# Kernel tuning notes

Hardware: AMD Instinct MI355X
Metric: run time of the kernel (lower is better)

The kernel has to match this reference:

```python
import jax, jax.numpy as jnp
import numpy as np

N = 100000       # nodes
E0 = 1600000     # random edges (self-loops appended -> E = E0 + N)
IN = 128         # input feature dim
H1, C1 = 8, 8    # conv1 heads, out channels per head
C2 = 64          # num_classes (conv2 out, heads=1)
NEG_SLOPE = 0.2


def gat_conv(x, src, dst, W, att_src, att_dst, bias, heads, out_ch, concat):
    """PyG-style GATConv (eval mode, no dropout). x: [N, F_in]."""
    n = x.shape[0]
    h = (x @ W).reshape(n, heads, out_ch)              # [N, H, C]
    a_src = jnp.sum(h * att_src, axis=-1)              # [N, H]
    a_dst = jnp.sum(h * att_dst, axis=-1)              # [N, H]
    e = jax.nn.leaky_relu(a_src[src] + a_dst[dst], NEG_SLOPE)  # [E, H]
    # segment softmax over edges grouped by destination node
    e_max = jax.ops.segment_max(e, dst, num_segments=n)
    ex = jnp.exp(e - e_max[dst])
    denom = jax.ops.segment_sum(ex, dst, num_segments=n)
    alpha = ex / denom[dst]                            # [E, H]
    msg = h[src] * alpha[:, :, None]                   # [E, H, C]
    out = jax.ops.segment_sum(msg, dst, num_segments=n)  # [N, H, C]
    out = out.reshape(n, heads * out_ch) if concat else out.mean(axis=1)
    return out + bias


def setup_inputs() -> dict:
    key = jax.random.key(0)
    ks = jax.random.split(key, 12)
    nodes = jnp.arange(N, dtype=jnp.int32)
    feat = jax.random.normal(ks[0], (N, IN), jnp.float32)
    src = jax.random.randint(ks[1], (E0,), 0, N, jnp.int32)
    dst = jax.random.randint(ks[2], (E0,), 0, N, jnp.int32)
    loop = jnp.arange(N, dtype=jnp.int32)
    edge_index = jnp.stack([jnp.concatenate([src, loop]),
                            jnp.concatenate([dst, loop])])  # [2, E]
    mask = jnp.ones((N,), bool)
    label = jax.random.randint(ks[3], (N,), 0, C2, jnp.int32)
    s = 0.1
    W1 = jax.random.normal(ks[4], (IN, H1 * C1), jnp.float32) * s
    att_src1 = jax.random.normal(ks[5], (H1, C1), jnp.float32) * s
    att_dst1 = jax.random.normal(ks[6], (H1, C1), jnp.float32) * s
    b1 = jnp.zeros((H1 * C1,), jnp.float32)
    W2 = jax.random.normal(ks[7], (H1 * C1, C2), jnp.float32) * s
    att_src2 = jax.random.normal(ks[8], (1, C2), jnp.float32) * s
    att_dst2 = jax.random.normal(ks[9], (1, C2), jnp.float32) * s
    b2 = jnp.zeros((C2,), jnp.float32)
    return {"nodes": nodes, "feat": feat, "edge_index": edge_index, "mask": mask,
            "label": label, "W1": W1, "att_src1": att_src1, "att_dst1": att_dst1,
            "b1": b1, "W2": W2, "att_src2": att_src2, "att_dst2": att_dst2, "b2": b2}


def reference(nodes, feat, edge_index, mask, label,
              W1, att_src1, att_dst1, b1, W2, att_src2, att_dst2, b2):
    src, dst = edge_index[0], edge_index[1]
    x = jax.nn.elu(gat_conv(feat, src, dst, W1, att_src1, att_dst1, b1,
                            H1, C1, concat=True))          # [N, 64]
    scores = gat_conv(x, src, dst, W2, att_src2, att_dst2, b2,
                      1, C2, concat=False)                  # [N, C2]
    logp = jax.nn.log_softmax(scores, axis=-1)
    nll = -jnp.take_along_axis(logp, label[:, None].astype(jnp.int32), axis=1)[:, 0]
    m = mask.astype(scores.dtype)
    loss = jnp.sum(nll * m) / jnp.sum(m)                    # masked mean CE
    pred = jnp.argmax(scores, axis=1)
    return loss, pred, label
```

## Files before the change

kernel.cpp:

```cpp
#include <hip/hip_runtime.h>
#include <cstdint>

#define NHEAD 8
#define D1 64
#define IN_F 128
#define NEG 0.2f
#define NBINS 256
#define BINS 1024
#define BSH 7
#define CHUNK 8192

__device__ __forceinline__ void fma4(float4& a, float s, const float4& v)
{
    a.x = fmaf(s, v.x, a.x); a.y = fmaf(s, v.y, a.y);
    a.z = fmaf(s, v.z, a.z); a.w = fmaf(s, v.w, a.w);
}

__global__ __launch_bounds__(256) void k_gemm1_hist(
    const float* __restrict__ feat,
    const float* __restrict__ W1,
    const float* __restrict__ att_s,
    const float* __restrict__ att_d,
    float* __restrict__ h1, float* __restrict__ a_src, float* __restrict__ a_dst,
    const int* __restrict__ dst, int* __restrict__ btot, int* __restrict__ bh,
    int N, int E, int GH)
{
    __shared__ float Wh[32 * 64];
    __shared__ float Fh[64 * 36];
    const int tid = threadIdx.x;

    if ((int)blockIdx.x < GH) {
        int* hist = (int*)Wh;
        for (int b = tid; b < BINS; b += 256) hist[b] = 0;
        __syncthreads();
        const int e0 = blockIdx.x * CHUNK;
        #pragma unroll
        for (int r = 0; r < 8; ++r) {
            int e = e0 + r * 1024 + tid * 4;
            if (e + 3 < E) {
                int4 d4 = *(const int4*)&dst[e];
                atomicAdd(&hist[d4.x >> BSH], 1);
                atomicAdd(&hist[d4.y >> BSH], 1);
                atomicAdd(&hist[d4.z >> BSH], 1);
                atomicAdd(&hist[d4.w >> BSH], 1);
            } else {
                for (int k = e; k < E && k < e + 4; ++k)
                    atomicAdd(&hist[dst[k] >> BSH], 1);
            }
        }
        __syncthreads();
        for (int b = tid; b < BINS; b += 256) {
            int c = hist[b];
            bh[(size_t)blockIdx.x * BINS + b] = c;
            if (c) atomicAdd(&btot[b * 16], c);
        }
        return;
    }

    const int tx = tid & 15, ty = tid >> 4;
    const int base = (blockIdx.x - GH) * 64;
    float4 acc0 = {0,0,0,0}, acc1 = {0,0,0,0}, acc2 = {0,0,0,0}, acc3 = {0,0,0,0};

    for (int p = 0; p < 4; ++p) {
        if (p) __syncthreads();
        for (int i = tid; i < 32 * 64; i += 256)
            Wh[i] = W1[p * 2048 + i];
        for (int i = tid; i < 64 * 32; i += 256) {
            int r = i >> 5, kk = i & 31;
            int n = base + r;
            Fh[r * 36 + kk] = (n < N) ? feat[(size_t)n * IN_F + p * 32 + kk] : 0.f;
        }
        __syncthreads();
        const float* wk = &Wh[4 * tx];
        const float* f0 = &Fh[(4 * ty + 0) * 36];
        const float* f1 = &Fh[(4 * ty + 1) * 36];
        const float* f2 = &Fh[(4 * ty + 2) * 36];
        const float* f3 = &Fh[(4 * ty + 3) * 36];
        #pragma unroll
        for (int kk = 0; kk < 32; kk += 4) {
            float4 fa = *(const float4*)&f0[kk];
            float4 fb = *(const float4*)&f1[kk];
            float4 fc = *(const float4*)&f2[kk];
            float4 fd = *(const float4*)&f3[kk];
            float4 w0 = *(const float4*)&wk[(kk + 0) * 64];
            float4 w1 = *(const float4*)&wk[(kk + 1) * 64];
            float4 w2 = *(const float4*)&wk[(kk + 2) * 64];
            float4 w3 = *(const float4*)&wk[(kk + 3) * 64];
            fma4(acc0, fa.x, w0); fma4(acc0, fa.y, w1); fma4(acc0, fa.z, w2); fma4(acc0, fa.w, w3);
            fma4(acc1, fb.x, w0); fma4(acc1, fb.y, w1); fma4(acc1, fb.z, w2); fma4(acc1, fb.w, w3);
            fma4(acc2, fc.x, w0); fma4(acc2, fc.y, w1); fma4(acc2, fc.z, w2); fma4(acc2, fc.w, w3);
            fma4(acc3, fd.x, w0); fma4(acc3, fd.y, w1); fma4(acc3, fd.z, w2); fma4(acc3, fd.w, w3);
        }
    }
    const float4 as4 = *(const float4*)&att_s[4 * tx];
    const float4 ad4 = *(const float4*)&att_d[4 * tx];
    float4 accs[4] = {acc0, acc1, acc2, acc3};
    #pragma unroll
    for (int i = 0; i < 4; ++i) {
        int n = base + 4 * ty + i;
        if (n < N) {
            *(float4*)&h1[(size_t)n * D1 + 4 * tx] = accs[i];
            float ps = accs[i].x * as4.x + accs[i].y * as4.y + accs[i].z * as4.z + accs[i].w * as4.w;
            float pd = accs[i].x * ad4.x + accs[i].y * ad4.y + accs[i].z * ad4.z + accs[i].w * ad4.w;
            ps += __shfl_xor(ps, 1);
            pd += __shfl_xor(pd, 1);
            if ((tx & 1) == 0) {
                a_src[n * NHEAD + (tx >> 1)] = ps;
                a_dst[n * NHEAD + (tx >> 1)] = pd;
            }
        }
    }
}

__device__ __forceinline__ int block_incl_scan(int v, int tid, int* lds4)
{
    int lane = tid & 63, w = tid >> 6;
    #pragma unroll
    for (int off = 1; off < 64; off <<= 1) {
        int t = __shfl_up(v, off);
        if (lane >= off) v += t;
    }
    if (lane == 63) lds4[w] = v;
    __syncthreads();
    int add = 0;
    #pragma unroll
    for (int i = 0; i < 4; ++i)
        if (i < w) add += lds4[i];
    __syncthreads();
    return v + add;
}

__global__ __launch_bounds__(256) void k_bscan(
    const int* __restrict__ btot, int* __restrict__ bbase, int* __restrict__ gcur,
    double* __restrict__ bins)
{
    __shared__ int lds4[4];
    const int tid = threadIdx.x;
    bins[tid] = 0.0;
    int c0 = btot[(4 * tid + 0) * 16];
    int c1 = btot[(4 * tid + 1) * 16];
    int c2 = btot[(4 * tid + 2) * 16];
    int c3 = btot[(4 * tid + 3) * 16];
    int v = c0 + c1 + c2 + c3;
    int incl = block_incl_scan(v, tid, lds4);
    int b0 = incl - v, b1 = b0 + c0, b2 = b1 + c1, b3 = b2 + c2;
    bbase[4 * tid + 0] = b0; gcur[(4 * tid + 0) * 16] = b0;
    bbase[4 * tid + 1] = b1; gcur[(4 * tid + 1) * 16] = b1;
    bbase[4 * tid + 2] = b2; gcur[(4 * tid + 2) * 16] = b2;
    bbase[4 * tid + 3] = b3; gcur[(4 * tid + 3) * 16] = b3;
}

__global__ __launch_bounds__(256) void k_scatter(
    const int* __restrict__ src, const int* __restrict__ dst,
    const int* __restrict__ bh, int* __restrict__ gcur,
    int* __restrict__ bucketed, int E)
{
    __shared__ int base[BINS], cur[BINS];
    const int tid = threadIdx.x;
    for (int b = tid; b < BINS; b += 256) {
        cur[b] = 0;
        int c = bh[(size_t)blockIdx.x * BINS + b];
        if (c) base[b] = atomicAdd(&gcur[b * 16], c);
    }
    __syncthreads();
    const int e0 = blockIdx.x * CHUNK;
    #pragma unroll
    for (int r = 0; r < 8; ++r) {
        int e = e0 + r * 1024 + tid * 4;
        if (e + 3 < E) {
            int4 d4 = *(const int4*)&dst[e];
            int4 s4 = *(const int4*)&src[e];
            int bx, rx;
            bx = d4.x >> BSH; rx = atomicAdd(&cur[bx], 1); bucketed[base[bx] + rx] = ((d4.x & 127) << 17) | s4.x;
            bx = d4.y >> BSH; rx = atomicAdd(&cur[bx], 1); bucketed[base[bx] + rx] = ((d4.y & 127) << 17) | s4.y;
            bx = d4.z >> BSH; rx = atomicAdd(&cur[bx], 1); bucketed[base[bx] + rx] = ((d4.z & 127) << 17) | s4.z;
            bx = d4.w >> BSH; rx = atomicAdd(&cur[bx], 1); bucketed[base[bx] + rx] = ((d4.w & 127) << 17) | s4.w;
        } else {
            for (int k = e; k < E && k < e + 4; ++k) {
                int d = dst[k];
                int bx = d >> BSH;
                int rx = atomicAdd(&cur[bx], 1);
                bucketed[base[bx] + rx] = ((d & 127) << 17) | src[k];
            }
        }
    }
}

__global__ __launch_bounds__(256) void k_seg(
    const int* __restrict__ btot, const int* __restrict__ bbase,
    const int* __restrict__ bucketed,
    int* __restrict__ deg, int* __restrict__ rowstart, int* __restrict__ srcs, int N)
{
    __shared__ int cnt[128], cur[128], lb[128];
    const int tid = threadIdx.x;
    const int b = blockIdx.x;
    const int gs = bbase[b];
    const int sz = btot[b * 16];
    if (tid < 128) { cnt[tid] = 0; cur[tid] = 0; }
    __syncthreads();
    for (int i = tid; i < sz; i += 256)
        atomicAdd(&cnt[bucketed[gs + i] >> 17], 1);
    __syncthreads();
    if (tid < 128) lb[tid] = cnt[tid];
    __syncthreads();
    #pragma unroll
    for (int off = 1; off < 128; off <<= 1) {
        int t = 0;
        if (tid < 128 && tid >= off) t = lb[tid - off];
        __syncthreads();
        if (tid < 128 && tid >= off) lb[tid] += t;
        __syncthreads();
    }
    if (tid < 128) {
        int ex = lb[tid] - cnt[tid];
        lb[tid] = ex;
        int d = b * 128 + tid;
        if (d < N) { deg[d] = cnt[tid]; rowstart[d] = gs + ex; }
    }
    __syncthreads();
    for (int i = tid; i < sz; i += 256) {
        int v = bucketed[gs + i];
        int d7 = v >> 17;
        int r = atomicAdd(&cur[d7], 1);
        srcs[gs + lb[d7] + r] = v & 0x1FFFF;
    }
}

__global__ __launch_bounds__(256) void k_agg1(
    const int* __restrict__ deg, const int* __restrict__ rowstart,
    const int* __restrict__ srcs,
    const float* __restrict__ a_s, const float* __restrict__ a_d,
    const float* __restrict__ h1, const float* __restrict__ b1,
    float* __restrict__ x, int N)
{
    __shared__ float sex[4][128];
    const int tid = threadIdx.x, w = tid >> 6, j = tid & 63;
    const int t = j & 15, q = j >> 4;
    const int n = blockIdx.x * 4 + w;
    if (n >= N) return;
    const int rlen = deg[n];
    const int row = rowstart[n];
    const float2 ad2 = *(const float2*)&a_d[n * NHEAD + 2 * q];
    const int h = t >> 1;
    float* sw = sex[w];
    float4 acc = {0.f, 0.f, 0.f, 0.f};
    float den = 0.f;
    bool v = (t < rlen);
    int   s  = v ? srcs[row + t] : 0;
    float2 a2 = v ? *(const float2*)&a_s[s * NHEAD + 2 * q] : make_float2(0.f, 0.f);
    for (int base = 0; base < rlen; base += 16) {
        bool vn = (base + 16 + t < rlen);
        int   sn  = vn ? srcs[row + base + 16 + t] : 0;
        float2 an = vn ? *(const float2*)&a_s[sn * NHEAD + 2 * q] : make_float2(0.f, 0.f);
        float e0 = 0.f, e1 = 0.f;
        if (v) {
            float x0 = a2.x + ad2.x; x0 = x0 > 0.f ? x0 : NEG * x0; e0 = __expf(x0);
            float x1 = a2.y + ad2.y; x1 = x1 > 0.f ? x1 : NEG * x1; e1 = __expf(x1);
        }
        *(float2*)&sw[t * 8 + 2 * q] = make_float2(e0, e1);
        asm volatile("s_waitcnt lgkmcnt(0)" ::: "memory");
        int mTot = rlen - base;
        if (4 * q < mTot) {
            int s0 = __shfl(s, 4 * q + 0), s1 = __shfl(s, 4 * q + 1);
            int s2 = __shfl(s, 4 * q + 2), s3 = __shfl(s, 4 * q + 3);
            float w0 = sw[(4 * q + 0) * 8 + h], w1 = sw[(4 * q + 1) * 8 + h];
            float w2 = sw[(4 * q + 2) * 8 + h], w3 = sw[(4 * q + 3) * 8 + h];
            float4 l0 = *(const float4*)&h1[(size_t)s0 * D1 + 4 * t];
            float4 l1 = *(const float4*)&h1[(size_t)s1 * D1 + 4 * t];
            float4 l2 = *(const float4*)&h1[(size_t)s2 * D1 + 4 * t];
            float4 l3 = *(const float4*)&h1[(size_t)s3 * D1 + 4 * t];
            fma4(acc, w0, l0); fma4(acc, w1, l1);
            fma4(acc, w2, l2); fma4(acc, w3, l3);
            den += (w0 + w1) + (w2 + w3);
        }
        asm volatile("s_waitcnt lgkmcnt(0)" ::: "memory");
        v = vn; s = sn; a2 = an;
    }
    acc.x += __shfl_xor(acc.x, 16); acc.y += __shfl_xor(acc.y, 16);
    acc.z += __shfl_xor(acc.z, 16); acc.w += __shfl_xor(acc.w, 16);
    den   += __shfl_xor(den, 16);
    acc.x += __shfl_xor(acc.x, 32); acc.y += __shfl_xor(acc.y, 32);
    acc.z += __shfl_xor(acc.z, 32); acc.w += __shfl_xor(acc.w, 32);
    den   += __shfl_xor(den, 32);
    if (q == 0) {
        float4 b = *(const float4*)&b1[4 * t];
        float4 o;
        o.x = acc.x / den + b.x; o.y = acc.y / den + b.y;
        o.z = acc.z / den + b.z; o.w = acc.w / den + b.w;
        o.x = o.x > 0.f ? o.x : expm1f(o.x);
        o.y = o.y > 0.f ? o.y : expm1f(o.y);
        o.z = o.z > 0.f ? o.z : expm1f(o.z);
        o.w = o.w > 0.f ? o.w : expm1f(o.w);
        *(float4*)&x[(size_t)n * D1 + 4 * t] = o;
    }
}

__global__ __launch_bounds__(256) void k_gemm2(
    const float* __restrict__ x,
    const float* __restrict__ W2,
    const float* __restrict__ att_s,
    const float* __restrict__ att_d,
    float* __restrict__ h2, float* __restrict__ a_src, float* __restrict__ a_dst,
    int N)
{
    __shared__ float Wh[64 * 64];
    __shared__ float Fh[64 * 68];
    const int tid = threadIdx.x;
    const int tx = tid & 15, ty = tid >> 4;
    const int base = blockIdx.x * 64;
    for (int i = tid; i < 64 * 64; i += 256)
        Wh[i] = W2[i];
    for (int i = tid; i < 64 * 64; i += 256) {
        int r = i >> 6, kk = i & 63;
        int n = base + r;
        Fh[r * 68 + kk] = (n < N) ? x[(size_t)n * 64 + kk] : 0.f;
    }
    __syncthreads();
    float4 acc0 = {0,0,0,0}, acc1 = {0,0,0,0}, acc2 = {0,0,0,0}, acc3 = {0,0,0,0};
    const float* wk = &Wh[4 * tx];
    const float* f0 = &Fh[(4 * ty + 0) * 68];
    const float* f1 = &Fh[(4 * ty + 1) * 68];
    const float* f2 = &Fh[(4 * ty + 2) * 68];
    const float* f3 = &Fh[(4 * ty + 3) * 68];
    #pragma unroll 4
    for (int kk = 0; kk < 64; kk += 4) {
        float4 fa = *(const float4*)&f0[kk];
        float4 fb = *(const float4*)&f1[kk];
        float4 fc = *(const float4*)&f2[kk];
        float4 fd = *(const float4*)&f3[kk];
        float4 w0 = *(const float4*)&wk[(kk + 0) * 64];
        float4 w1 = *(const float4*)&wk[(kk + 1) * 64];
        float4 w2 = *(const float4*)&wk[(kk + 2) * 64];
        float4 w3 = *(const float4*)&wk[(kk + 3) * 64];
        fma4(acc0, fa.x, w0); fma4(acc0, fa.y, w1); fma4(acc0, fa.z, w2); fma4(acc0, fa.w, w3);
        fma4(acc1, fb.x, w0); fma4(acc1, fb.y, w1); fma4(acc1, fb.z, w2); fma4(acc1, fb.w, w3);
        fma4(acc2, fc.x, w0); fma4(acc2, fc.y, w1); fma4(acc2, fc.z, w2); fma4(acc2, fc.w, w3);
        fma4(acc3, fd.x, w0); fma4(acc3, fd.y, w1); fma4(acc3, fd.z, w2); fma4(acc3, fd.w, w3);
    }
    const float4 as4 = *(const float4*)&att_s[4 * tx];
    const float4 ad4 = *(const float4*)&att_d[4 * tx];
    float4 accs[4] = {acc0, acc1, acc2, acc3};
    #pragma unroll
    for (int i = 0; i < 4; ++i) {
        int n = base + 4 * ty + i;
        if (n < N) {
            *(float4*)&h2[(size_t)n * 64 + 4 * tx] = accs[i];
            float ps = accs[i].x * as4.x + accs[i].y * as4.y + accs[i].z * as4.z + accs[i].w * as4.w;
            float pd = accs[i].x * ad4.x + accs[i].y * ad4.y + accs[i].z * ad4.z + accs[i].w * ad4.w;
            ps += __shfl_xor(ps, 1); pd += __shfl_xor(pd, 1);
            ps += __shfl_xor(ps, 2); pd += __shfl_xor(pd, 2);
            ps += __shfl_xor(ps, 4); pd += __shfl_xor(pd, 4);
            ps += __shfl_xor(ps, 8); pd += __shfl_xor(pd, 8);
            if (tx == 0) { a_src[n] = ps; a_dst[n] = pd; }
        }
    }
}

__global__ __launch_bounds__(256) void k_agg2(
    const int* __restrict__ deg, const int* __restrict__ rowstart,
    const int* __restrict__ srcs,
    const float* __restrict__ a_s, const float* __restrict__ a_d,
    const float* __restrict__ h2, const float* __restrict__ b2,
    const int* __restrict__ label,
    float* __restrict__ dout, double* __restrict__ bins, int N)
{
    __shared__ int2 sx[4][64];
    __shared__ float snll[16];
    const int tid = threadIdx.x, w = tid >> 6, j = tid & 63;
    const int t = j & 15, g16 = j & 0x30;
    const int n = blockIdx.x * 16 + (tid >> 4);
    if (tid < 16) snll[tid] = 0.f;
    __syncthreads();
    const bool valid = (n < N);
    const int rlen = valid ? deg[n] : 0;
    const int row  = valid ? rowstart[n] : 0;
    const float ad = valid ? a_d[n] : 0.f;
    float4 acc = {0.f, 0.f, 0.f, 0.f};
    float den = 0.f;
    for (int base = 0; base < rlen; base += 16) {
        int m = rlen - base; if (m > 16) m = 16;
        int myS = 0; float ex = 0.f;
        if (t < m) {
            myS = srcs[row + base + t];
            float v = a_s[myS] + ad;
            v = v > 0.f ? v : NEG * v;
            ex = __expf(v);
        }
        float ds = ex;
        ds += __shfl_xor(ds, 1); ds += __shfl_xor(ds, 2);
        ds += __shfl_xor(ds, 4); ds += __shfl_xor(ds, 8);
        den += ds;
        sx[w][j] = make_int2(myS, __float_as_int(ex));
        asm volatile("s_waitcnt lgkmcnt(0)" ::: "memory");
        for (int kb = 0; kb < m; kb += 4) {
            int2 p0 = sx[w][g16 | (kb + 0)];
            int2 p1 = sx[w][g16 | (kb + 1)];
            int2 p2 = sx[w][g16 | (kb + 2)];
            int2 p3 = sx[w][g16 | (kb + 3)];
            float4 l0 = *(const float4*)&h2[(size_t)p0.x * 64 + 4 * t];
            float4 l1 = *(const float4*)&h2[(size_t)p1.x * 64 + 4 * t];
            float4 l2 = *(const float4*)&h2[(size_t)p2.x * 64 + 4 * t];
            float4 l3 = *(const float4*)&h2[(size_t)p3.x * 64 + 4 * t];
            fma4(acc, __int_as_float(p0.y), l0);
            fma4(acc, __int_as_float(p1.y), l1);
            fma4(acc, __int_as_float(p2.y), l2);
            fma4(acc, __int_as_float(p3.y), l3);
        }
        asm volatile("s_waitcnt lgkmcnt(0)" ::: "memory");
    }
    float4 b = *(const float4*)&b2[4 * t];
    float4 sc;
    sc.x = acc.x / den + b.x; sc.y = acc.y / den + b.y;
    sc.z = acc.z / den + b.z; sc.w = acc.w / den + b.w;
    float mv = sc.x; int mi = 4 * t;
    if (sc.y > mv) { mv = sc.y; mi = 4 * t + 1; }
    if (sc.z > mv) { mv = sc.z; mi = 4 * t + 2; }
    if (sc.w > mv) { mv = sc.w; mi = 4 * t + 3; }
    #pragma unroll
    for (int off = 1; off < 16; off <<= 1) {
        float ov = __shfl_xor(mv, off);
        int oi = __shfl_xor(mi, off);
        if (ov > mv || (ov == mv && oi < mi)) { mv = ov; mi = oi; }
    }
    float se = __expf(sc.x - mv) + __expf(sc.y - mv) + __expf(sc.z - mv) + __expf(sc.w - mv);
    #pragma unroll
    for (int off = 1; off < 16; off <<= 1) se += __shfl_xor(se, off);
    int lab = valid ? label[n] : 0;
    int comp = lab & 3;
    float cl = comp == 0 ? sc.x : comp == 1 ? sc.y : comp == 2 ? sc.z : sc.w;
    float sl = __shfl(cl, g16 | (lab >> 2));
    if (t == 0 && valid) {
        snll[tid >> 4] = mv + logf(se) - sl;
        dout[1 + n] = (float)mi;
        dout[1 + (size_t)N + n] = (float)lab;
    }
    __syncthreads();
    if (tid == 0) {
        double bs = 0.0;
        #pragma unroll
        for (int i = 0; i < 16; ++i) bs += (double)snll[i];
        atomicAdd(&bins[blockIdx.x & (NBINS - 1)], bs);
    }
}

__global__ __launch_bounds__(256) void k_loss(
    const double* __restrict__ bins, float* __restrict__ dout, int N)
{
    __shared__ double sw[4];
    const int tid = threadIdx.x;
    double v = bins[tid];
    #pragma unroll
    for (int off = 1; off < 64; off <<= 1) v += __shfl_xor(v, off);
    if ((tid & 63) == 0) sw[tid >> 6] = v;
    __syncthreads();
    if (tid == 0)
        dout[0] = (float)((sw[0] + sw[1] + sw[2] + sw[3]) / (double)N);
}

extern "C" void kernel_launch(void* const* d_in, const int* in_sizes, int n_in,
                              void* d_out, int out_size, void* d_ws, size_t ws_size,
                              hipStream_t stream)
{
    const float* feat   = (const float*)d_in[1];
    const int*   edge   = (const int*)d_in[2];
    const int*   label  = (const int*)d_in[4];
    const float* W1     = (const float*)d_in[5];
    const float* att_s1 = (const float*)d_in[6];
    const float* att_d1 = (const float*)d_in[7];
    const float* b1     = (const float*)d_in[8];
    const float* W2     = (const float*)d_in[9];
    const float* att_s2 = (const float*)d_in[10];
    const float* att_d2 = (const float*)d_in[11];
    const float* b2     = (const float*)d_in[12];

    const int N = in_sizes[0];
    const int E = in_sizes[2] / 2;
    const int* src = edge;
    const int* dst = edge + E;

    float* bufA = (float*)d_ws;
    float* bufB = bufA + (size_t)N * 64;
    float* a_s1 = bufB + (size_t)N * 64;
    float* a_d1 = a_s1 + (size_t)N * 8;
    int*   deg  = (int*)(a_d1 + (size_t)N * 8);
    int*   rowstart = deg + N;
    int*   srcs = rowstart + N;
    double* bins = (double*)(((uintptr_t)(srcs + E) + 7) & ~(uintptr_t)7);

    int* bucketed = (int*)bufB;
    int* btot  = bucketed + E;
    int* gcur  = btot + BINS * 16;
    int* bbase = gcur + BINS * 16;
    int* bh    = bbase + BINS;

    float* a_s2 = a_s1;
    float* a_d2 = a_s1 + N;

    float* out = (float*)d_out;

    const int GH    = (E + CHUNK - 1) / CHUNK;
    const int G1    = (N + 63) / 64;
    const int NBUCK = (N + 127) / 128;

    hipMemsetAsync(btot, 0, (size_t)BINS * 16 * sizeof(int), stream);

    k_gemm1_hist<<<GH + G1, 256, 0, stream>>>(feat, W1, att_s1, att_d1,
                                              bufA, a_s1, a_d1,
                                              dst, btot, bh, N, E, GH);
    k_bscan  <<<1, 256, 0, stream>>>(btot, bbase, gcur, bins);
    k_scatter<<<GH, 256, 0, stream>>>(src, dst, bh, gcur, bucketed, E);
    k_seg    <<<NBUCK, 256, 0, stream>>>(btot, bbase, bucketed, deg, rowstart, srcs, N);

    k_agg1 <<<(N + 3) / 4, 256, 0, stream>>>(deg, rowstart, srcs, a_s1, a_d1,
                                             bufA, b1, bufB, N);
    k_gemm2<<<G1, 256, 0, stream>>>(bufB, W2, att_s2, att_d2, bufA, a_s2, a_d2, N);
    k_agg2 <<<(N + 15) / 16, 256, 0, stream>>>(deg, rowstart, srcs, a_s2, a_d2,
                                               bufA, b2, label, out, bins, N);
    k_loss <<<1, 256, 0, stream>>>(bins, out, N);
}
```

Measured before the change: 390.3 us.

## Spread GEMM1 tiles across CSR-build kernels and simplify agg1 weight computation

The layer-1 GEMM tiles are split into four portions and fused into the histogram, bucket-scan, scatter and segment kernels as extra blocks. The single-block scan and the atomic-bound sort stages then share the GPU with compute work instead of leaving CUs idle. Separately, k_agg1 drops the LDS-staged, software-prefetched exp weights and has each lane load its sources and compute its own exp directly. This removes LDS traffic and waitcnt barriers but adds redundant a_s loads and exp work per lane, and loses the prefetch pipelining.

```diff
diff --git a/kernel.cpp b/kernel.cpp
--- a/kernel.cpp
+++ b/kernel.cpp
@@ -16,49 +16,18 @@
     a.z = fmaf(s, v.z, a.z); a.w = fmaf(s, v.w, a.w);
 }
 
-__global__ __launch_bounds__(256) void k_gemm1_hist(
-    const float* __restrict__ feat,
-    const float* __restrict__ W1,
-    const float* __restrict__ att_s,
-    const float* __restrict__ att_d,
+__device__ __forceinline__ void gemm1_tile(
+    int gb,
+    const float* __restrict__ feat, const float* __restrict__ W1,
+    const float* __restrict__ att_s, const float* __restrict__ att_d,
     float* __restrict__ h1, float* __restrict__ a_src, float* __restrict__ a_dst,
-    const int* __restrict__ dst, int* __restrict__ btot, int* __restrict__ bh,
-    int N, int E, int GH)
+    int N)
 {
     __shared__ float Wh[32 * 64];
     __shared__ float Fh[64 * 36];
     const int tid = threadIdx.x;
-
-    if ((int)blockIdx.x < GH) {
-        int* hist = (int*)Wh;
-        for (int b = tid; b < BINS; b += 256) hist[b] = 0;
-        __syncthreads();
-        const int e0 = blockIdx.x * CHUNK;
-        #pragma unroll
-        for (int r = 0; r < 8; ++r) {
-            int e = e0 + r * 1024 + tid * 4;
-            if (e + 3 < E) {
-                int4 d4 = *(const int4*)&dst[e];
-                atomicAdd(&hist[d4.x >> BSH], 1);
-                atomicAdd(&hist[d4.y >> BSH], 1);
-                atomicAdd(&hist[d4.z >> BSH], 1);
-                atomicAdd(&hist[d4.w >> BSH], 1);
-            } else {
-                for (int k = e; k < E && k < e + 4; ++k)
-                    atomicAdd(&hist[dst[k] >> BSH], 1);
-            }
-        }
-        __syncthreads();
-        for (int b = tid; b < BINS; b += 256) {
-            int c = hist[b];
-            bh[(size_t)blockIdx.x * BINS + b] = c;
-            if (c) atomicAdd(&btot[b * 16], c);
-        }
-        return;
-    }
-
     const int tx = tid & 15, ty = tid >> 4;
-    const int base = (blockIdx.x - GH) * 64;
+    const int base = gb * 64;
     float4 acc0 = {0,0,0,0}, acc1 = {0,0,0,0}, acc2 = {0,0,0,0}, acc3 = {0,0,0,0};
 
     for (int p = 0; p < 4; ++p) {
@@ -112,6 +81,44 @@
     }
 }
 
+__global__ __launch_bounds__(256) void k_hist_g1(
+    const float* __restrict__ feat, const float* __restrict__ W1,
+    const float* __restrict__ att_s, const float* __restrict__ att_d,
+    float* __restrict__ h1, float* __restrict__ a_src, float* __restrict__ a_dst,
+    const int* __restrict__ dst, int* __restrict__ btot, int* __restrict__ bh,
+    int N, int E, int GH)
+{
+    const int tid = threadIdx.x;
+    if ((int)blockIdx.x < GH) {
+        __shared__ int hist[BINS];
+        for (int b = tid; b < BINS; b += 256) hist[b] = 0;
+        __syncthreads();
+        const int e0 = blockIdx.x * CHUNK;
+        #pragma unroll
+        for (int r = 0; r < 8; ++r) {
+            int e = e0 + r * 1024 + tid * 4;
+            if (e + 3 < E) {
+                int4 d4 = *(const int4*)&dst[e];
+                atomicAdd(&hist[d4.x >> BSH], 1);
+                atomicAdd(&hist[d4.y >> BSH], 1);
+                atomicAdd(&hist[d4.z >> BSH], 1);
+                atomicAdd(&hist[d4.w >> BSH], 1);
+            } else {
+                for (int k = e; k < E && k < e + 4; ++k)
+                    atomicAdd(&hist[dst[k] >> BSH], 1);
+            }
+        }
+        __syncthreads();
+        for (int b = tid; b < BINS; b += 256) {
+            int c = hist[b];
+            bh[(size_t)blockIdx.x * BINS + b] = c;
+            if (c) atomicAdd(&btot[b * 16], c);
+        }
+        return;
+    }
+    gemm1_tile(blockIdx.x - GH, feat, W1, att_s, att_d, h1, a_src, a_dst, N);
+}
+
 __device__ __forceinline__ int block_incl_scan(int v, int tid, int* lds4)
 {
     int lane = tid & 63, w = tid >> 6;
@@ -130,100 +137,122 @@
     return v + add;
 }
 
-__global__ __launch_bounds__(256) void k_bscan(
+__global__ __launch_bounds__(256) void k_bscan_g1(
+    const float* __restrict__ feat, const float* __restrict__ W1,
+    const float* __restrict__ att_s, const float* __restrict__ att_d,
+    float* __restrict__ h1, float* __restrict__ a_src, float* __restrict__ a_dst,
     const int* __restrict__ btot, int* __restrict__ bbase, int* __restrict__ gcur,
-    double* __restrict__ bins)
-{
-    __shared__ int lds4[4];
-    const int tid = threadIdx.x;
-    bins[tid] = 0.0;
-    int c0 = btot[(4 * tid + 0) * 16];
-    int c1 = btot[(4 * tid + 1) * 16];
-    int c2 = btot[(4 * tid + 2) * 16];
-    int c3 = btot[(4 * tid + 3) * 16];
-    int v = c0 + c1 + c2 + c3;
-    int incl = block_incl_scan(v, tid, lds4);
-    int b0 = incl - v, b1 = b0 + c0, b2 = b1 + c1, b3 = b2 + c2;
-    bbase[4 * tid + 0] = b0; gcur[(4 * tid + 0) * 16] = b0;
-    bbase[4 * tid + 1] = b1; gcur[(4 * tid + 1) * 16] = b1;
-    bbase[4 * tid + 2] = b2; gcur[(4 * tid + 2) * 16] = b2;
-    bbase[4 * tid + 3] = b3; gcur[(4 * tid + 3) * 16] = b3;
-}
-
-__global__ __launch_bounds__(256) void k_scatter(
+    double* __restrict__ bins, int N, int goff)
+{
+    if (blockIdx.x == 0) {
+        __shared__ int lds4[4];
+        const int tid = threadIdx.x;
+        bins[tid] = 0.0;
+        int c0 = btot[(4 * tid + 0) * 16];
+        int c1 = btot[(4 * tid + 1) * 16];
+        int c2 = btot[(4 * tid + 2) * 16];
+        int c3 = btot[(4 * tid + 3) * 16];
+        int v = c0 + c1 + c2 + c3;
+        int incl = block_incl_scan(v, tid, lds4);
+        int b0 = incl - v, b1 = b0 + c0, b2 = b1 + c1, b3 = b2 + c2;
+        bbase[4 * tid + 0] = b0; gcur[(4 * tid + 0) * 16] = b0;
+        bbase[4 * tid + 1] = b1; gcur[(4 * tid + 1) * 16] = b1;
+        bbase[4 * tid + 2] = b2; gcur[(4 * tid + 2) * 16] = b2;
+        bbase[4 * tid + 3] = b3; gcur[(4 * tid + 3) * 16] = b3;
+        return;
+    }
+    gemm1_tile(goff + (int)blockIdx.x - 1, feat, W1, att_s, att_d, h1, a_src, a_dst, N);
+}
+
+__global__ __launch_bounds__(256) void k_scatter_g1(
+    const float* __restrict__ feat, const float* __restrict__ W1,
+    const float* __restrict__ att_s, const float* __restrict__ att_d,
+    float* __restrict__ h1, float* __restrict__ a_src, float* __restrict__ a_dst,
     const int* __restrict__ src, const int* __restrict__ dst,
     const int* __restrict__ bh, int* __restrict__ gcur,
-    int* __restrict__ bucketed, int E)
-{
-    __shared__ int base[BINS], cur[BINS];
+    int* __restrict__ bucketed, int N, int E, int GH, int goff)
+{
     const int tid = threadIdx.x;
-    for (int b = tid; b < BINS; b += 256) {
-        cur[b] = 0;
-        int c = bh[(size_t)blockIdx.x * BINS + b];
-        if (c) base[b] = atomicAdd(&gcur[b * 16], c);
-    }
-    __syncthreads();
-    const int e0 = blockIdx.x * CHUNK;
-    #pragma unroll
-    for (int r = 0; r < 8; ++r) {
-        int e = e0 + r * 1024 + tid * 4;
-        if (e + 3 < E) {
-            int4 d4 = *(const int4*)&dst[e];
-            int4 s4 = *(const int4*)&src[e];
-            int bx, rx;
-            bx = d4.x >> BSH; rx = atomicAdd(&cur[bx], 1); bucketed[base[bx] + rx] = ((d4.x & 127) << 17) | s4.x;
-            bx = d4.y >> BSH; rx = atomicAdd(&cur[bx], 1); bucketed[base[bx] + rx] = ((d4.y & 127) << 17) | s4.y;
-            bx = d4.z >> BSH; rx = atomicAdd(&cur[bx], 1); bucketed[base[bx] + rx] = ((d4.z & 127) << 17) | s4.z;
-            bx = d4.w >> BSH; rx = atomicAdd(&cur[bx], 1); bucketed[base[bx] + rx] = ((d4.w & 127) << 17) | s4.w;
-        } else {
-            for (int k = e; k < E && k < e + 4; ++k) {
-                int d = dst[k];
-                int bx = d >> BSH;
-                int rx = atomicAdd(&cur[bx], 1);
-                bucketed[base[bx] + rx] = ((d & 127) << 17) | src[k];
+    if ((int)blockIdx.x < GH) {
+        __shared__ int base[BINS], cur[BINS];
+        for (int b = tid; b < BINS; b += 256) {
+            cur[b] = 0;
+            int c = bh[(size_t)blockIdx.x * BINS + b];
+            if (c) base[b] = atomicAdd(&gcur[b * 16], c);
+        }
+        __syncthreads();
+        const int e0 = blockIdx.x * CHUNK;
+        #pragma unroll
+        for (int r = 0; r < 8; ++r) {
+            int e = e0 + r * 1024 + tid * 4;
+            if (e + 3 < E) {
+                int4 d4 = *(const int4*)&dst[e];
+                int4 s4 = *(const int4*)&src[e];
+                int bx, rx;
+                bx = d4.x >> BSH; rx = atomicAdd(&cur[bx], 1); bucketed[base[bx] + rx] = ((d4.x & 127) << 17) | s4.x;
+                bx = d4.y >> BSH; rx = atomicAdd(&cur[bx], 1); bucketed[base[bx] + rx] = ((d4.y & 127) << 17) | s4.y;
+                bx = d4.z >> BSH; rx = atomicAdd(&cur[bx], 1); bucketed[base[bx] + rx] = ((d4.z & 127) << 17) | s4.z;
+                bx = d4.w >> BSH; rx = atomicAdd(&cur[bx], 1); bucketed[base[bx] + rx] = ((d4.w & 127) << 17) | s4.w;
+            } else {
+                for (int k = e; k < E && k < e + 4; ++k) {
+                    int d = dst[k];
+                    int bx = d >> BSH;
+                    int rx = atomicAdd(&cur[bx], 1);
+                    bucketed[base[bx] + rx] = ((d & 127) << 17) | src[k];
+                }
             }
         }
-    }
-}
-
-__global__ __launch_bounds__(256) void k_seg(
+        return;
+    }
+    gemm1_tile(goff + (int)blockIdx.x - GH, feat, W1, att_s, att_d, h1, a_src, a_dst, N);
+}
+
+__global__ __launch_bounds__(256) void k_seg_g1(
+    const float* __restrict__ feat, const float* __restrict__ W1,
+    const float* __restrict__ att_s, const float* __restrict__ att_d,
+    float* __restrict__ h1, float* __restrict__ a_src, float* __restrict__ a_dst,
     const int* __restrict__ btot, const int* __restrict__ bbase,
     const int* __restrict__ bucketed,
-    int* __restrict__ deg, int* __restrict__ rowstart, int* __restrict__ srcs, int N)
-{
-    __shared__ int cnt[128], cur[128], lb[128];
+    int* __restrict__ deg, int* __restrict__ rowstart, int* __restrict__ srcs,
+    int N, int NBUCK, int goff)
+{
     const int tid = threadIdx.x;
-    const int b = blockIdx.x;
-    const int gs = bbase[b];
-    const int sz = btot[b * 16];
-    if (tid < 128) { cnt[tid] = 0; cur[tid] = 0; }
-    __syncthreads();
-    for (int i = tid; i < sz; i += 256)
-        atomicAdd(&cnt[bucketed[gs + i] >> 17], 1);
-    __syncthreads();
-    if (tid < 128) lb[tid] = cnt[tid];
-    __syncthreads();
-    #pragma unroll
-    for (int off = 1; off < 128; off <<= 1) {
-        int t = 0;
-        if (tid < 128 && tid >= off) t = lb[tid - off];
-        __syncthreads();
-        if (tid < 128 && tid >= off) lb[tid] += t;
-        __syncthreads();
-    }
-    if (tid < 128) {
-        int ex = lb[tid] - cnt[tid];
-        lb[tid] = ex;
-        int d = b * 128 + tid;
-        if (d < N) { deg[d] = cnt[tid]; rowstart[d] = gs + ex; }
-    }
-    __syncthreads();
-    for (int i = tid; i < sz; i += 256) {
-        int v = bucketed[gs + i];
-        int d7 = v >> 17;
-        int r = atomicAdd(&cur[d7], 1);
-        srcs[gs + lb[d7] + r] = v & 0x1FFFF;
-    }
+    if ((int)blockIdx.x < NBUCK) {
+        __shared__ int cnt[128], cur[128], lb[128];
+        const int b = blockIdx.x;
+        const int gs = bbase[b];
+        const int sz = btot[b * 16];
+        if (tid < 128) { cnt[tid] = 0; cur[tid] = 0; }
+        __syncthreads();
+        for (int i = tid; i < sz; i += 256)
+            atomicAdd(&cnt[bucketed[gs + i] >> 17], 1);
+        __syncthreads();
+        if (tid < 128) lb[tid] = cnt[tid];
+        __syncthreads();
+        #pragma unroll
+        for (int off = 1; off < 128; off <<= 1) {
+            int t = 0;
+            if (tid < 128 && tid >= off) t = lb[tid - off];
+            __syncthreads();
+            if (tid < 128 && tid >= off) lb[tid] += t;
+            __syncthreads();
+        }
+        if (tid < 128) {
+            int ex = lb[tid] - cnt[tid];
+            lb[tid] = ex;
+            int d = b * 128 + tid;
+            if (d < N) { deg[d] = cnt[tid]; rowstart[d] = gs + ex; }
+        }
+        __syncthreads();
+        for (int i = tid; i < sz; i += 256) {
+            int v = bucketed[gs + i];
+            int d7 = v >> 17;
+            int r = atomicAdd(&cur[d7], 1);
+            srcs[gs + lb[d7] + r] = v & 0x1FFFF;
+        }
+        return;
+    }
+    gemm1_tile(goff + (int)blockIdx.x - NBUCK, feat, W1, att_s, att_d, h1, a_src, a_dst, N);
 }
 
 __global__ __launch_bounds__(256) void k_agg1(
@@ -233,48 +262,45 @@
     const float* __restrict__ h1, const float* __restrict__ b1,
     float* __restrict__ x, int N)
 {
-    __shared__ float sex[4][128];
     const int tid = threadIdx.x, w = tid >> 6, j = tid & 63;
     const int t = j & 15, q = j >> 4;
     const int n = blockIdx.x * 4 + w;
     if (n >= N) return;
     const int rlen = deg[n];
     const int row = rowstart[n];
-    const float2 ad2 = *(const float2*)&a_d[n * NHEAD + 2 * q];
     const int h = t >> 1;
-    float* sw = sex[w];
+    const float ad = a_d[n * NHEAD + h];
     float4 acc = {0.f, 0.f, 0.f, 0.f};
     float den = 0.f;
-    bool v = (t < rlen);
-    int   s  = v ? srcs[row + t] : 0;
-    float2 a2 = v ? *(const float2*)&a_s[s * NHEAD + 2 * q] : make_float2(0.f, 0.f);
     for (int base = 0; base < rlen; base += 16) {
-        bool vn = (base + 16 + t < rlen);
-        int   sn  = vn ? srcs[row + base + 16 + t] : 0;
-        float2 an = vn ? *(const float2*)&a_s[sn * NHEAD + 2 * q] : make_float2(0.f, 0.f);
-        float e0 = 0.f, e1 = 0.f;
-        if (v) {
-            float x0 = a2.x + ad2.x; x0 = x0 > 0.f ? x0 : NEG * x0; e0 = __expf(x0);
-            float x1 = a2.y + ad2.y; x1 = x1 > 0.f ? x1 : NEG * x1; e1 = __expf(x1);
-        }
-        *(float2*)&sw[t * 8 + 2 * q] = make_float2(e0, e1);
-        asm volatile("s_waitcnt lgkmcnt(0)" ::: "memory");
         int mTot = rlen - base;
         if (4 * q < mTot) {
-            int s0 = __shfl(s, 4 * q + 0), s1 = __shfl(s, 4 * q + 1);
-            int s2 = __shfl(s, 4 * q + 2), s3 = __shfl(s, 4 * q + 3);
-            float w0 = sw[(4 * q + 0) * 8 + h], w1 = sw[(4 * q + 1) * 8 + h];
-            float w2 = sw[(4 * q + 2) * 8 + h], w3 = sw[(4 * q + 3) * 8 + h];
+            int rem = mTot - 4 * q;
+            int i0 = row + base + 4 * q;
+            int s0 = srcs[i0];
+            int s1 = rem > 1 ? srcs[i0 + 1] : 0;
+            int s2 = rem > 2 ? srcs[i0 + 2] : 0;
+            int s3 = rem > 3 ? srcs[i0 + 3] : 0;
+            float v0 = a_s[s0 * NHEAD + h] + ad;
+            float v1 = a_s[s1 * NHEAD + h] + ad;
+            float v2 = a_s[s2 * NHEAD + h] + ad;
+            float v3 = a_s[s3 * NHEAD + h] + ad;
+            v0 = v0 > 0.f ? v0 : NEG * v0;
+            v1 = v1 > 0.f ? v1 : NEG * v1;
+            v2 = v2 > 0.f ? v2 : NEG * v2;
+            v3 = v3 > 0.f ? v3 : NEG * v3;
+            float e0 = __expf(v0);
+            float e1 = rem > 1 ? __expf(v1) : 0.f;
+            float e2 = rem > 2 ? __expf(v2) : 0.f;
+            float e3 = rem > 3 ? __expf(v3) : 0.f;
             float4 l0 = *(const float4*)&h1[(size_t)s0 * D1 + 4 * t];
             float4 l1 = *(const float4*)&h1[(size_t)s1 * D1 + 4 * t];
             float4 l2 = *(const float4*)&h1[(size_t)s2 * D1 + 4 * t];
             float4 l3 = *(const float4*)&h1[(size_t)s3 * D1 + 4 * t];
-            fma4(acc, w0, l0); fma4(acc, w1, l1);
-            fma4(acc, w2, l2); fma4(acc, w3, l3);
-            den += (w0 + w1) + (w2 + w3);
-        }
-        asm volatile("s_waitcnt lgkmcnt(0)" ::: "memory");
-        v = vn; s = sn; a2 = an;
+            fma4(acc, e0, l0); fma4(acc, e1, l1);
+            fma4(acc, e2, l2); fma4(acc, e3, l3);
+            den += (e0 + e1) + (e2 + e3);
+        }
     }
     acc.x += __shfl_xor(acc.x, 16); acc.y += __shfl_xor(acc.y, 16);
     acc.z += __shfl_xor(acc.z, 16); acc.w += __shfl_xor(acc.w, 16);
@@ -502,14 +528,28 @@
     const int G1    = (N + 63) / 64;
     const int NBUCK = (N + 127) / 128;
 
+    const int GA = (int)((long)G1 * 40 / 100);
+    const int GB = (int)((long)G1 * 10 / 100);
+    const int GC = (int)((long)G1 * 30 / 100);
+    const int GD = G1 - GA - GB - GC;
+
     hipMemsetAsync(btot, 0, (size_t)BINS * 16 * sizeof(int), stream);
 
-    k_gemm1_hist<<<GH + G1, 256, 0, stream>>>(feat, W1, att_s1, att_d1,
+    k_hist_g1   <<<GH + GA, 256, 0, stream>>>(feat, W1, att_s1, att_d1,
                                               bufA, a_s1, a_d1,
                                               dst, btot, bh, N, E, GH);
-    k_bscan  <<<1, 256, 0, stream>>>(btot, bbase, gcur, bins);
-    k_scatter<<<GH, 256, 0, stream>>>(src, dst, bh, gcur, bucketed, E);
-    k_seg    <<<NBUCK, 256, 0, stream>>>(btot, bbase, bucketed, deg, rowstart, srcs, N);
+    k_bscan_g1  <<<1 + GB, 256, 0, stream>>>(feat, W1, att_s1, att_d1,
+                                             bufA, a_s1, a_d1,
+                                             btot, bbase, gcur, bins, N, GA);
+    k_scatter_g1<<<GH + GC, 256, 0, stream>>>(feat, W1, att_s1, att_d1,
+                                              bufA, a_s1, a_d1,
+                                              src, dst, bh, gcur, bucketed,
+                                              N, E, GH, GA + GB);
+    k_seg_g1    <<<NBUCK + GD, 256, 0, stream>>>(feat, W1, att_s1, att_d1,
+                                                 bufA, a_s1, a_d1,
+                                                 btot, bbase, bucketed,
+                                                 deg, rowstart, srcs,
+                                                 N, NBUCK, GA + GB + GC);
 
     k_agg1 <<<(N + 3) / 4, 256, 0, stream>>>(deg, rowstart, srcs, a_s1, a_d1,
                                              bufA, b1, bufB, N);
```

After: 419.9 us. +7.6%, slower.
